# Kernel optimization log

Hardware: AMD Instinct MI355X
Metric: run time of the kernel (lower is better)

Reference implementation:

```python
import jax, jax.numpy as jnp
import numpy as np

B, D_IN, D_HID, D_OUT, E, TOP_K = 4096, 1024, 4096, 1024, 8, 2


def setup_inputs() -> dict:
    key = jax.random.key(0)
    ks = jax.random.split(key, 7)
    s_in = 1.0 / np.sqrt(D_IN)
    s_hid = 1.0 / np.sqrt(D_HID)
    return {
        "x": jax.random.normal(ks[0], (B, D_IN), jnp.float32),
        "Wg": jax.random.uniform(ks[1], (D_IN, E), jnp.float32, -s_in, s_in),
        "bg": jax.random.uniform(ks[2], (E,), jnp.float32, -s_in, s_in),
        "W1": jax.random.uniform(ks[3], (E, D_IN, D_HID), jnp.float32, -s_in, s_in),
        "b1": jax.random.uniform(ks[4], (E, D_HID), jnp.float32, -s_in, s_in),
        "W2": jax.random.uniform(ks[5], (E, D_HID, D_OUT), jnp.float32, -s_hid, s_hid),
        "b2": jax.random.uniform(ks[6], (E, D_OUT), jnp.float32, -s_hid, s_hid),
    }


def reference(x, Wg, bg, W1, b1, W2, b2):
    # Gating: [B, E]
    gate_logits = x @ Wg + bg
    # Top-k routing (values sorted descending, same as torch.topk)
    topk_logits, topk_idx = jax.lax.top_k(gate_logits, TOP_K)  # [B, K]
    topk_w = jax.nn.softmax(topk_logits, axis=-1)  # [B, K]

    # Dense per-expert FFN for all tokens (reference form of grouped GEMM)
    h = jax.nn.relu(jnp.einsum("bi,eih->beh", x, W1) + b1[None])  # [B, E, H]
    y = jnp.einsum("beh,eho->beo", h, W2) + b2[None]              # [B, E, O]

    # Gather selected experts' outputs and combine with routing weights
    y_sel = jnp.take_along_axis(y, topk_idx[:, :, None], axis=1)  # [B, K, O]
    output = jnp.sum(topk_w[:, :, None] * y_sel, axis=1)          # [B, O]

    # Load-balance auxiliary loss
    gates = jax.nn.softmax(gate_logits, axis=-1)
    expert_usage = gates.mean(axis=0)
    load_balance_loss = E * jnp.sum(expert_usage ** 2)
    return output, load_balance_loss
```

## Files before the change

kernel.cpp:

```cpp
#include <hip/hip_runtime.h>
#include <hip/hip_fp16.h>

#define BTOK  4096
#define D_IN  1024
#define D_HID 4096
#define D_OUT 1024
#define NE    8
#define PT_MAX 72
#define P_MAX  9216
#define HHALF  2048
#define KT1    32
#define NT1    16
#define KT2    64
#define NT2    8
#define GB     256

typedef _Float16 half8 __attribute__((ext_vector_type(8)));
typedef _Float16 half4v __attribute__((ext_vector_type(4)));
typedef float    floatx4 __attribute__((ext_vector_type(4)));


__device__ __forceinline__ void g2l16(const void* g, void* s) {
    __builtin_amdgcn_global_load_lds((const __attribute__((address_space(1))) void*)g,
                                     (__attribute__((address_space(3))) void*)s, 16, 0, 0);
}

__global__ __launch_bounds__(256)
void gating_kernel(const float* __restrict__ x, const float* __restrict__ Wg,
                   const float* __restrict__ bg,
                   int* __restrict__ t2i, float* __restrict__ t2w,
                   int* __restrict__ pcnt, float* __restrict__ pusage) {
    __shared__ float wgT[NE * 1024];
    __shared__ float susage[NE];
    __shared__ int   scnt[NE];
    int tid = threadIdx.x;
    if (tid < NE) { susage[tid] = 0.f; scnt[tid] = 0; }
    #pragma unroll
    for (int k = 0; k < 8192; k += 256) {
        int idx = k + tid;
        wgT[(idx & 7) * 1024 + (idx >> 3)] = Wg[idx];
    }
    __syncthreads();
    int wv = tid >> 6, lane = tid & 63;
    for (int tt = 0; tt < 4; ++tt) {
        int t = blockIdx.x * 16 + wv * 4 + tt;
        double part[NE];
        #pragma unroll
        for (int e = 0; e < NE; ++e) part[e] = 0.0;
        #pragma unroll
        for (int j = 0; j < 16; ++j) {
            int i = j * 64 + lane;
            double xv = (double)x[(size_t)t * D_IN + i];
            #pragma unroll
            for (int e = 0; e < NE; ++e) part[e] += xv * (double)wgT[e * 1024 + i];
        }
        #pragma unroll
        for (int e = 0; e < NE; ++e) {
            #pragma unroll
            for (int s = 32; s > 0; s >>= 1) part[e] += __shfl_xor(part[e], s, 64);
        }
        if (lane == 0) {
            float l[NE];
            #pragma unroll
            for (int e = 0; e < NE; ++e) l[e] = (float)part[e] + bg[e];
            float M = l[0];
            #pragma unroll
            for (int e = 1; e < NE; ++e) M = fmaxf(M, l[e]);
            float s = 0.f, g[NE];
            #pragma unroll
            for (int e = 0; e < NE; ++e) { g[e] = __expf(l[e] - M); s += g[e]; }
            float inv = 1.f / s;
            #pragma unroll
            for (int e = 0; e < NE; ++e) atomicAdd(&susage[e], g[e] * inv);
            int i0 = 0; float b0 = l[0];
            #pragma unroll
            for (int e = 1; e < NE; ++e) if (l[e] > b0) { b0 = l[e]; i0 = e; }
            int i1 = -1; float b1v = -1e30f;
            #pragma unroll
            for (int e = 0; e < NE; ++e) if (e != i0 && l[e] > b1v) { b1v = l[e]; i1 = e; }
            float w0 = 1.f / (1.f + expf(b1v - b0));
            t2i[2 * t] = i0; t2i[2 * t + 1] = i1;
            t2w[2 * t] = w0; t2w[2 * t + 1] = 1.f - w0;
            atomicAdd(&scnt[i0], 1);
            atomicAdd(&scnt[i1], 1);
        }
    }
    __syncthreads();
    if (tid < NE) {
        pcnt[blockIdx.x * NE + tid] = scnt[tid];
        pusage[blockIdx.x * NE + tid] = susage[tid];
    }
}

__global__ void scan_kernel(const int* __restrict__ pcnt, const float* __restrict__ pusage,
                            int* __restrict__ meta, float* __restrict__ out_loss) {
    int lane = threadIdx.x;
    int e = lane & 7, b0 = lane >> 3;
    int c = 0; float u = 0.f;
    for (int b = b0; b < GB; b += 8) { c += pcnt[b * 8 + e]; u += pusage[b * 8 + e]; }
    #pragma unroll
    for (int s = 8; s < 64; s <<= 1) { c += __shfl_xor(c, s, 64); u += __shfl_xor(u, s, 64); }
    int cAll[NE]; float uAll[NE];
    #pragma unroll
    for (int q = 0; q < NE; ++q) { cAll[q] = __shfl(c, q, 64); uAll[q] = __shfl(u, q, 64); }
    if (lane == 0) {
        int* cnt = meta; int* cursor = meta + 8; int* offs = meta + 16;
        int* tile2e = meta + 24; int* ntiles = meta + 96;
        int run = 0;
        for (int q = 0; q < NE; ++q) {
            cnt[q] = cAll[q];
            offs[q] = run; cursor[q] = run;
            int ntl = (cAll[q] + 127) >> 7;
            int tb = run >> 7;
            for (int i = 0; i < ntl; ++i) tile2e[tb + i] = q;
            run += ntl << 7;
        }
        ntiles[0] = run >> 7;
        float loss = 0.f;
        for (int q = 0; q < NE; ++q) { float uu = uAll[q] / (float)BTOK; loss += uu * uu; }
        out_loss[0] = (float)NE * loss;
    }
}

__global__ void fill_kernel(int* __restrict__ ptok) {
    ptok[blockIdx.x * 256 + threadIdx.x] = 0;
}

__global__ void scatter_kernel(const int* __restrict__ t2i, int* __restrict__ cursor,
                               int* __restrict__ ptok, int* __restrict__ pslot) {
    __shared__ int lcnt[NE], base[NE];
    int tid = threadIdx.x;
    if (tid < NE) lcnt[tid] = 0;
    __syncthreads();
    int t = blockIdx.x * 256 + tid;
    int e0 = t2i[2 * t], e1 = t2i[2 * t + 1];
    int l0 = atomicAdd(&lcnt[e0], 1);
    int l1 = atomicAdd(&lcnt[e1], 1);
    __syncthreads();
    if (tid < NE) base[tid] = atomicAdd(&cursor[tid], lcnt[tid]);
    __syncthreads();
    int s0 = base[e0] + l0, s1 = base[e1] + l1;
    ptok[s0] = t; ptok[s1] = t;
    pslot[2 * t] = s0; pslot[2 * t + 1] = s1;
}

__global__ void gather_x_kernel(const float* __restrict__ x, const int* __restrict__ ptok,
                                _Float16* __restrict__ xt) {
    int k0 = blockIdx.x, ptile = blockIdx.y;
    int t = threadIdx.x;
    int m = t >> 1, kb = (t & 1) * 16;
    int tok = ptok[ptile * 128 + m];
    const float* src = x + (size_t)tok * D_IN + k0 * 32 + kb;
    float4 v0 = *(const float4*)(src);
    float4 v1 = *(const float4*)(src + 4);
    float4 v2 = *(const float4*)(src + 8);
    float4 v3 = *(const float4*)(src + 12);
    half8 o0, o1;
    o0[0]=(_Float16)v0.x; o0[1]=(_Float16)v0.y; o0[2]=(_Float16)v0.z; o0[3]=(_Float16)v0.w;
    o0[4]=(_Float16)v1.x; o0[5]=(_Float16)v1.y; o0[6]=(_Float16)v1.z; o0[7]=(_Float16)v1.w;
    o1[0]=(_Float16)v2.x; o1[1]=(_Float16)v2.y; o1[2]=(_Float16)v2.z; o1[3]=(_Float16)v2.w;
    o1[4]=(_Float16)v3.x; o1[5]=(_Float16)v3.y; o1[6]=(_Float16)v3.z; o1[7]=(_Float16)v3.w;
    _Float16* dst = xt + ((size_t)ptile * KT1 + k0) * 4096 + t * 16;
    *(half8*)dst = o0;
    *(half8*)(dst + 8) = o1;
}

__global__ void wtile_kernel(const float* __restrict__ W, _Float16* __restrict__ Wt,
                             int Ktot, int Ntot, int k_off, int n_off, int KT, int NT) {
    int k0 = blockIdx.x, ntb = blockIdx.y, e = blockIdx.z;
    int t = threadIdx.x;
    int nl = t >> 1, kb = (t & 1) * 16;
    const float* src = W + ((size_t)e * Ktot + k_off + k0 * 32 + kb) * Ntot
                         + n_off + ntb * 128 + nl;
    float v[16];
    #pragma unroll
    for (int j = 0; j < 16; ++j) v[j] = src[(size_t)j * Ntot];
    half8 o0, o1;
    #pragma unroll
    for (int j = 0; j < 8; ++j) { o0[j] = (_Float16)v[j]; o1[j] = (_Float16)v[j + 8]; }
    _Float16* dst = Wt + (((size_t)e * NT + ntb) * KT + k0) * 4096 + t * 16;
    *(half8*)dst = o0;
    *(half8*)(dst + 8) = o1;
}

__global__ __launch_bounds__(256)
void gemm1_kernel(const _Float16* __restrict__ xt, const _Float16* __restrict__ W1t,
                  const float* __restrict__ b1, _Float16* __restrict__ ht,
                  const int* __restrict__ meta, int n_off) {
    int ptile = blockIdx.x;
    if (ptile >= meta[96]) return;
    int nt = blockIdx.y;
    int e = meta[24 + ptile];

    __shared__ __align__(16) _Float16 Asm[128 * 32];
    __shared__ __align__(16) _Float16 Bsm[128 * 32];

    int tid = threadIdx.x;
    int wave = tid >> 6, lane = tid & 63;
    const _Float16* Abase = xt + (size_t)ptile * KT1 * 4096;
    const _Float16* Bbase = W1t + ((size_t)(e * NT1 + nt) * KT1) * 4096;
    int stg = wave * 512 + lane * 8;

    floatx4 acc[4][4] = {};
    int lr = lane & 15, lq = lane >> 4;
    int wm = (wave & 1) * 64, wn = (wave >> 1) * 64;

    for (int k0 = 0; k0 < KT1; ++k0) {
        __syncthreads();
        const _Float16* aG = Abase + (size_t)k0 * 4096 + stg;
        const _Float16* bG = Bbase + (size_t)k0 * 4096 + stg;
        g2l16(aG,        &Asm[wave * 512]);
        g2l16(aG + 2048, &Asm[wave * 512 + 2048]);
        g2l16(bG,        &Bsm[wave * 512]);
        g2l16(bG + 2048, &Bsm[wave * 512 + 2048]);
        __syncthreads();
        half8 af[4], bf[4];
        #pragma unroll
        for (int f = 0; f < 4; ++f) {
            af[f] = *(const half8*)&Asm[(wm + f * 16 + lr) * 32 + lq * 8];
            bf[f] = *(const half8*)&Bsm[(wn + f * 16 + lr) * 32 + lq * 8];
        }
        #pragma unroll
        for (int mf = 0; mf < 4; ++mf)
            #pragma unroll
            for (int nf = 0; nf < 4; ++nf)
                acc[mf][nf] = __builtin_amdgcn_mfma_f32_16x16x32_f16(af[mf], bf[nf], acc[mf][nf], 0, 0, 0);
    }

    const float* b1e = b1 + (size_t)e * D_HID + n_off;
    #pragma unroll
    for (int mf = 0; mf < 4; ++mf) {
        #pragma unroll
        for (int v = 0; v < 4; ++v) {
            int m = wm + mf * 16 + lq * 4 + v;
            #pragma unroll
            for (int nf = 0; nf < 4; ++nf) {
                int hl = nt * 128 + wn + nf * 16 + lr;
                float val = acc[mf][nf][v] + b1e[hl];
                ht[((size_t)ptile * KT2 + (hl >> 5)) * 4096 + m * 32 + (hl & 31)]
                    = (_Float16)fmaxf(val, 0.f);
            }
        }
    }
}

__global__ __launch_bounds__(256)
void gemm2_kernel(const _Float16* __restrict__ ht, const _Float16* __restrict__ W2t,
                  _Float16* __restrict__ y, const int* __restrict__ meta) {
    int ptile = blockIdx.x;
    if (ptile >= meta[96]) return;
    int nt = blockIdx.y;
    int e = meta[24 + ptile];

    __shared__ __align__(16) _Float16 Asm[128 * 32];
    __shared__ __align__(16) _Float16 Bsm[128 * 32];

    int tid = threadIdx.x;
    int wave = tid >> 6, lane = tid & 63;
    const _Float16* Abase = ht + (size_t)ptile * KT2 * 4096;
    const _Float16* Bbase = W2t + ((size_t)(e * NT2 + nt) * KT2) * 4096;
    int stg = wave * 512 + lane * 8;

    floatx4 acc[4][4] = {};
    int lr = lane & 15, lq = lane >> 4;
    int wm = (wave & 1) * 64, wn = (wave >> 1) * 64;

    for (int k0 = 0; k0 < KT2; ++k0) {
        __syncthreads();
        const _Float16* aG = Abase + (size_t)k0 * 4096 + stg;
        const _Float16* bG = Bbase + (size_t)k0 * 4096 + stg;
        g2l16(aG,        &Asm[wave * 512]);
        g2l16(aG + 2048, &Asm[wave * 512 + 2048]);
        g2l16(bG,        &Bsm[wave * 512]);
        g2l16(bG + 2048, &Bsm[wave * 512 + 2048]);
        __syncthreads();
        half8 af[4], bf[4];
        #pragma unroll
        for (int f = 0; f < 4; ++f) {
            af[f] = *(const half8*)&Asm[(wm + f * 16 + lr) * 32 + lq * 8];
            bf[f] = *(const half8*)&Bsm[(wn + f * 16 + lr) * 32 + lq * 8];
        }
        #pragma unroll
        for (int mf = 0; mf < 4; ++mf)
            #pragma unroll
            for (int nf = 0; nf < 4; ++nf)
                acc[mf][nf] = __builtin_amdgcn_mfma_f32_16x16x32_f16(af[mf], bf[nf], acc[mf][nf], 0, 0, 0);
    }

    #pragma unroll
    for (int mf = 0; mf < 4; ++mf) {
        #pragma unroll
        for (int v = 0; v < 4; ++v) {
            int m = wm + mf * 16 + lq * 4 + v;
            #pragma unroll
            for (int nf = 0; nf < 4; ++nf) {
                int c = nt * 128 + wn + nf * 16 + lr;
                y[(size_t)(ptile * 128 + m) * D_OUT + c] = (_Float16)acc[mf][nf][v];
            }
        }
    }
}

__global__ void combine_kernel(const _Float16* __restrict__ yA, const _Float16* __restrict__ yB,
                               const float* __restrict__ b2, const int* __restrict__ t2i,
                               const float* __restrict__ t2w, const int* __restrict__ pslot,
                               float* __restrict__ out) {
    int t = blockIdx.x;
    int c = threadIdx.x * 4;
    int e0 = t2i[2 * t], e1 = t2i[2 * t + 1];
    float w0 = t2w[2 * t], w1 = t2w[2 * t + 1];
    size_t s0 = (size_t)pslot[2 * t] * D_OUT + c;
    size_t s1 = (size_t)pslot[2 * t + 1] * D_OUT + c;
    half4v a0 = *(const half4v*)(yA + s0);
    half4v b0 = *(const half4v*)(yB + s0);
    half4v a1 = *(const half4v*)(yA + s1);
    half4v b1v = *(const half4v*)(yB + s1);
    float4 bias0 = *(const float4*)(b2 + (size_t)e0 * D_OUT + c);
    float4 bias1 = *(const float4*)(b2 + (size_t)e1 * D_OUT + c);
    float4 o;
    o.x = w0 * ((float)a0[0] + (float)b0[0] + bias0.x) + w1 * ((float)a1[0] + (float)b1v[0] + bias1.x);
    o.y = w0 * ((float)a0[1] + (float)b0[1] + bias0.y) + w1 * ((float)a1[1] + (float)b1v[1] + bias1.y);
    o.z = w0 * ((float)a0[2] + (float)b0[2] + bias0.z) + w1 * ((float)a1[2] + (float)b1v[2] + bias1.z);
    o.w = w0 * ((float)a0[3] + (float)b0[3] + bias0.w) + w1 * ((float)a1[3] + (float)b1v[3] + bias1.w);
    *(float4*)(out + (size_t)t * D_OUT + c) = o;
}

extern "C" void kernel_launch(void* const* d_in, const int* in_sizes, int n_in,
                              void* d_out, int out_size, void* d_ws, size_t ws_size,
                              hipStream_t stream) {
    const float* x  = (const float*)d_in[0];
    const float* Wg = (const float*)d_in[1];
    const float* bg = (const float*)d_in[2];
    const float* W1 = (const float*)d_in[3];
    const float* b1 = (const float*)d_in[4];
    const float* W2 = (const float*)d_in[5];
    const float* b2 = (const float*)d_in[6];
    float* out = (float*)d_out;

    char* ws = (char*)d_ws;
    _Float16* xt     = (_Float16*)(ws);
    _Float16* Wt     = (_Float16*)(ws + 18874368ull);
    _Float16* ht     = (_Float16*)(ws + 52428800ull);
    _Float16* yA     = (_Float16*)(ws + 90177536ull);
    _Float16* yB     = (_Float16*)(ws + 109051904ull);
    int*      t2i    = (int*)(ws + 127926272ull);
    float*    t2w    = (float*)(ws + 127959040ull);
    int*      ptok   = (int*)(ws + 127991808ull);
    int*      pslot  = (int*)(ws + 128028672ull);
    int*      meta   = (int*)(ws + 128061440ull);
    int*      pcnt   = (int*)(ws + 128061952ull);
    float*    pusage = (float*)(ws + 128070144ull);
    int* cursor = meta + 8;

    hipMemsetAsync(meta, 0, 512, stream);

    gating_kernel<<<GB, 256, 0, stream>>>(x, Wg, bg, t2i, t2w, pcnt, pusage);
    scan_kernel<<<1, 64, 0, stream>>>(pcnt, pusage, meta, out + (size_t)BTOK * D_OUT);
    fill_kernel<<<36, 256, 0, stream>>>(ptok);
    scatter_kernel<<<16, 256, 0, stream>>>(t2i, cursor, ptok, pslot);
    gather_x_kernel<<<dim3(KT1, PT_MAX), 256, 0, stream>>>(x, ptok, xt);

    wtile_kernel<<<dim3(KT1, NT1, 8), 256, 0, stream>>>(W1, Wt, D_IN, D_HID, 0, 0, KT1, NT1);
    gemm1_kernel<<<dim3(PT_MAX, NT1), 256, 0, stream>>>(xt, Wt, b1, ht, meta, 0);
    wtile_kernel<<<dim3(KT2, NT2, 8), 256, 0, stream>>>(W2, Wt, D_HID, D_OUT, 0, 0, KT2, NT2);
    gemm2_kernel<<<dim3(PT_MAX, NT2), 256, 0, stream>>>(ht, Wt, yA, meta);

    wtile_kernel<<<dim3(KT1, NT1, 8), 256, 0, stream>>>(W1, Wt, D_IN, D_HID, 0, HHALF, KT1, NT1);
    gemm1_kernel<<<dim3(PT_MAX, NT1), 256, 0, stream>>>(xt, Wt, b1, ht, meta, HHALF);
    wtile_kernel<<<dim3(KT2, NT2, 8), 256, 0, stream>>>(W2, Wt, D_HID, D_OUT, HHALF, 0, KT2, NT2);
    gemm2_kernel<<<dim3(PT_MAX, NT2), 256, 0, stream>>>(ht, Wt, yB, meta);

    combine_kernel<<<BTOK, 256, 0, stream>>>(yA, yB, b2, t2i, t2w, pslot, out);
}
```

Before: 585.2 us.

## Double-buffer GEMM LDS tiles and merge split hidden-dimension passes

```diff
diff --git a/kernel.cpp b/kernel.cpp
--- a/kernel.cpp
+++ b/kernel.cpp
@@ -8,12 +8,11 @@
 #define NE    8
 #define PT_MAX 72
 #define P_MAX  9216
-#define HHALF  2048
-#define KT1    32
-#define NT1    16
-#define KT2    64
-#define NT2    8
-#define GB     256
+#define KT1   32
+#define NT1M  32
+#define KT2M  128
+#define NT2   8
+#define GB    256
 
 typedef _Float16 half8 __attribute__((ext_vector_type(8)));
 typedef _Float16 half4v __attribute__((ext_vector_type(4)));
@@ -166,12 +165,11 @@
 }
 
 __global__ void wtile_kernel(const float* __restrict__ W, _Float16* __restrict__ Wt,
-                             int Ktot, int Ntot, int k_off, int n_off, int KT, int NT) {
+                             int Ktot, int Ntot, int KT, int NT) {
     int k0 = blockIdx.x, ntb = blockIdx.y, e = blockIdx.z;
     int t = threadIdx.x;
     int nl = t >> 1, kb = (t & 1) * 16;
-    const float* src = W + ((size_t)e * Ktot + k_off + k0 * 32 + kb) * Ntot
-                         + n_off + ntb * 128 + nl;
+    const float* src = W + ((size_t)e * Ktot + k0 * 32 + kb) * Ntot + ntb * 128 + nl;
     float v[16];
     #pragma unroll
     for (int j = 0; j < 16; ++j) v[j] = src[(size_t)j * Ntot];
@@ -183,51 +181,63 @@
     *(half8*)(dst + 8) = o1;
 }
 
-__global__ __launch_bounds__(256)
+__global__ __launch_bounds__(256, 3)
 void gemm1_kernel(const _Float16* __restrict__ xt, const _Float16* __restrict__ W1t,
                   const float* __restrict__ b1, _Float16* __restrict__ ht,
-                  const int* __restrict__ meta, int n_off) {
+                  const int* __restrict__ meta) {
     int ptile = blockIdx.x;
     if (ptile >= meta[96]) return;
     int nt = blockIdx.y;
     int e = meta[24 + ptile];
 
-    __shared__ __align__(16) _Float16 Asm[128 * 32];
-    __shared__ __align__(16) _Float16 Bsm[128 * 32];
+    __shared__ __align__(16) _Float16 Asm[2][128 * 32];
+    __shared__ __align__(16) _Float16 Bsm[2][128 * 32];
 
     int tid = threadIdx.x;
     int wave = tid >> 6, lane = tid & 63;
     const _Float16* Abase = xt + (size_t)ptile * KT1 * 4096;
-    const _Float16* Bbase = W1t + ((size_t)(e * NT1 + nt) * KT1) * 4096;
+    const _Float16* Bbase = W1t + ((size_t)(e * NT1M + nt) * KT1) * 4096;
     int stg = wave * 512 + lane * 8;
 
     floatx4 acc[4][4] = {};
     int lr = lane & 15, lq = lane >> 4;
     int wm = (wave & 1) * 64, wn = (wave >> 1) * 64;
 
+    g2l16(Abase + stg,        &Asm[0][wave * 512]);
+    g2l16(Abase + stg + 2048, &Asm[0][wave * 512 + 2048]);
+    g2l16(Bbase + stg,        &Bsm[0][wave * 512]);
+    g2l16(Bbase + stg + 2048, &Bsm[0][wave * 512 + 2048]);
+    __syncthreads();
+
+    int ct = 0;
     for (int k0 = 0; k0 < KT1; ++k0) {
-        __syncthreads();
-        const _Float16* aG = Abase + (size_t)k0 * 4096 + stg;
-        const _Float16* bG = Bbase + (size_t)k0 * 4096 + stg;
-        g2l16(aG,        &Asm[wave * 512]);
-        g2l16(aG + 2048, &Asm[wave * 512 + 2048]);
-        g2l16(bG,        &Bsm[wave * 512]);
-        g2l16(bG + 2048, &Bsm[wave * 512 + 2048]);
-        __syncthreads();
+        if (k0 + 1 < KT1) {
+            const _Float16* aG = Abase + (size_t)(k0 + 1) * 4096 + stg;
+            const _Float16* bG = Bbase + (size_t)(k0 + 1) * 4096 + stg;
+            int nb = ct ^ 1;
+            g2l16(aG,        &Asm[nb][wave * 512]);
+            g2l16(aG + 2048, &Asm[nb][wave * 512 + 2048]);
+            g2l16(bG,        &Bsm[nb][wave * 512]);
+            g2l16(bG + 2048, &Bsm[nb][wave * 512 + 2048]);
+        }
+        const _Float16* As = Asm[ct];
+        const _Float16* Bs = Bsm[ct];
         half8 af[4], bf[4];
         #pragma unroll
         for (int f = 0; f < 4; ++f) {
-            af[f] = *(const half8*)&Asm[(wm + f * 16 + lr) * 32 + lq * 8];
-            bf[f] = *(const half8*)&Bsm[(wn + f * 16 + lr) * 32 + lq * 8];
+            af[f] = *(const half8*)&As[(wm + f * 16 + lr) * 32 + lq * 8];
+            bf[f] = *(const half8*)&Bs[(wn + f * 16 + lr) * 32 + lq * 8];
         }
         #pragma unroll
         for (int mf = 0; mf < 4; ++mf)
             #pragma unroll
             for (int nf = 0; nf < 4; ++nf)
                 acc[mf][nf] = __builtin_amdgcn_mfma_f32_16x16x32_f16(af[mf], bf[nf], acc[mf][nf], 0, 0, 0);
-    }
-
-    const float* b1e = b1 + (size_t)e * D_HID + n_off;
+        __syncthreads();
+        ct ^= 1;
+    }
+
+    const float* b1e = b1 + (size_t)e * D_HID;
     #pragma unroll
     for (int mf = 0; mf < 4; ++mf) {
         #pragma unroll
@@ -237,14 +247,14 @@
             for (int nf = 0; nf < 4; ++nf) {
                 int hl = nt * 128 + wn + nf * 16 + lr;
                 float val = acc[mf][nf][v] + b1e[hl];
-                ht[((size_t)ptile * KT2 + (hl >> 5)) * 4096 + m * 32 + (hl & 31)]
+                ht[((size_t)ptile * KT2M + (hl >> 5)) * 4096 + m * 32 + (hl & 31)]
                     = (_Float16)fmaxf(val, 0.f);
             }
         }
     }
 }
 
-__global__ __launch_bounds__(256)
+__global__ __launch_bounds__(256, 3)
 void gemm2_kernel(const _Float16* __restrict__ ht, const _Float16* __restrict__ W2t,
                   _Float16* __restrict__ y, const int* __restrict__ meta) {
     int ptile = blockIdx.x;
@@ -252,39 +262,51 @@
     int nt = blockIdx.y;
     int e = meta[24 + ptile];
 
-    __shared__ __align__(16) _Float16 Asm[128 * 32];
-    __shared__ __align__(16) _Float16 Bsm[128 * 32];
+    __shared__ __align__(16) _Float16 Asm[2][128 * 32];
+    __shared__ __align__(16) _Float16 Bsm[2][128 * 32];
 
     int tid = threadIdx.x;
     int wave = tid >> 6, lane = tid & 63;
-    const _Float16* Abase = ht + (size_t)ptile * KT2 * 4096;
-    const _Float16* Bbase = W2t + ((size_t)(e * NT2 + nt) * KT2) * 4096;
+    const _Float16* Abase = ht + (size_t)ptile * KT2M * 4096;
+    const _Float16* Bbase = W2t + ((size_t)(e * NT2 + nt) * KT2M) * 4096;
     int stg = wave * 512 + lane * 8;
 
     floatx4 acc[4][4] = {};
     int lr = lane & 15, lq = lane >> 4;
     int wm = (wave & 1) * 64, wn = (wave >> 1) * 64;
 
-    for (int k0 = 0; k0 < KT2; ++k0) {
-        __syncthreads();
-        const _Float16* aG = Abase + (size_t)k0 * 4096 + stg;
-        const _Float16* bG = Bbase + (size_t)k0 * 4096 + stg;
-        g2l16(aG,        &Asm[wave * 512]);
-        g2l16(aG + 2048, &Asm[wave * 512 + 2048]);
-        g2l16(bG,        &Bsm[wave * 512]);
-        g2l16(bG + 2048, &Bsm[wave * 512 + 2048]);
-        __syncthreads();
+    g2l16(Abase + stg,        &Asm[0][wave * 512]);
+    g2l16(Abase + stg + 2048, &Asm[0][wave * 512 + 2048]);
+    g2l16(Bbase + stg,        &Bsm[0][wave * 512]);
+    g2l16(Bbase + stg + 2048, &Bsm[0][wave * 512 + 2048]);
+    __syncthreads();
+
+    int ct = 0;
+    for (int k0 = 0; k0 < KT2M; ++k0) {
+        if (k0 + 1 < KT2M) {
+            const _Float16* aG = Abase + (size_t)(k0 + 1) * 4096 + stg;
+            const _Float16* bG = Bbase + (size_t)(k0 + 1) * 4096 + stg;
+            int nb = ct ^ 1;
+            g2l16(aG,        &Asm[nb][wave * 512]);
+            g2l16(aG + 2048, &Asm[nb][wave * 512 + 2048]);
+            g2l16(bG,        &Bsm[nb][wave * 512]);
+            g2l16(bG + 2048, &Bsm[nb][wave * 512 + 2048]);
+        }
+        const _Float16* As = Asm[ct];
+        const _Float16* Bs = Bsm[ct];
         half8 af[4], bf[4];
         #pragma unroll
         for (int f = 0; f < 4; ++f) {
-            af[f] = *(const half8*)&Asm[(wm + f * 16 + lr) * 32 + lq * 8];
-            bf[f] = *(const half8*)&Bsm[(wn + f * 16 + lr) * 32 + lq * 8];
+            af[f] = *(const half8*)&As[(wm + f * 16 + lr) * 32 + lq * 8];
+            bf[f] = *(const half8*)&Bs[(wn + f * 16 + lr) * 32 + lq * 8];
         }
         #pragma unroll
         for (int mf = 0; mf < 4; ++mf)
             #pragma unroll
             for (int nf = 0; nf < 4; ++nf)
                 acc[mf][nf] = __builtin_amdgcn_mfma_f32_16x16x32_f16(af[mf], bf[nf], acc[mf][nf], 0, 0, 0);
+        __syncthreads();
+        ct ^= 1;
     }
 
     #pragma unroll
@@ -301,27 +323,24 @@
     }
 }
 
-__global__ void combine_kernel(const _Float16* __restrict__ yA, const _Float16* __restrict__ yB,
-                               const float* __restrict__ b2, const int* __restrict__ t2i,
-                               const float* __restrict__ t2w, const int* __restrict__ pslot,
-                               float* __restrict__ out) {
+__global__ void combine_kernel(const _Float16* __restrict__ y, const float* __restrict__ b2,
+                               const int* __restrict__ t2i, const float* __restrict__ t2w,
+                               const int* __restrict__ pslot, float* __restrict__ out) {
     int t = blockIdx.x;
     int c = threadIdx.x * 4;
     int e0 = t2i[2 * t], e1 = t2i[2 * t + 1];
     float w0 = t2w[2 * t], w1 = t2w[2 * t + 1];
     size_t s0 = (size_t)pslot[2 * t] * D_OUT + c;
     size_t s1 = (size_t)pslot[2 * t + 1] * D_OUT + c;
-    half4v a0 = *(const half4v*)(yA + s0);
-    half4v b0 = *(const half4v*)(yB + s0);
-    half4v a1 = *(const half4v*)(yA + s1);
-    half4v b1v = *(const half4v*)(yB + s1);
+    half4v a0 = *(const half4v*)(y + s0);
+    half4v a1 = *(const half4v*)(y + s1);
     float4 bias0 = *(const float4*)(b2 + (size_t)e0 * D_OUT + c);
     float4 bias1 = *(const float4*)(b2 + (size_t)e1 * D_OUT + c);
     float4 o;
-    o.x = w0 * ((float)a0[0] + (float)b0[0] + bias0.x) + w1 * ((float)a1[0] + (float)b1v[0] + bias1.x);
-    o.y = w0 * ((float)a0[1] + (float)b0[1] + bias0.y) + w1 * ((float)a1[1] + (float)b1v[1] + bias1.y);
-    o.z = w0 * ((float)a0[2] + (float)b0[2] + bias0.z) + w1 * ((float)a1[2] + (float)b1v[2] + bias1.z);
-    o.w = w0 * ((float)a0[3] + (float)b0[3] + bias0.w) + w1 * ((float)a1[3] + (float)b1v[3] + bias1.w);
+    o.x = w0 * ((float)a0[0] + bias0.x) + w1 * ((float)a1[0] + bias1.x);
+    o.y = w0 * ((float)a0[1] + bias0.y) + w1 * ((float)a1[1] + bias1.y);
+    o.z = w0 * ((float)a0[2] + bias0.z) + w1 * ((float)a1[2] + bias1.z);
+    o.w = w0 * ((float)a0[3] + bias0.w) + w1 * ((float)a1[3] + bias1.w);
     *(float4*)(out + (size_t)t * D_OUT + c) = o;
 }
 
@@ -339,17 +358,17 @@
 
     char* ws = (char*)d_ws;
     _Float16* xt     = (_Float16*)(ws);
-    _Float16* Wt     = (_Float16*)(ws + 18874368ull);
-    _Float16* ht     = (_Float16*)(ws + 52428800ull);
-    _Float16* yA     = (_Float16*)(ws + 90177536ull);
-    _Float16* yB     = (_Float16*)(ws + 109051904ull);
-    int*      t2i    = (int*)(ws + 127926272ull);
-    float*    t2w    = (float*)(ws + 127959040ull);
-    int*      ptok   = (int*)(ws + 127991808ull);
-    int*      pslot  = (int*)(ws + 128028672ull);
-    int*      meta   = (int*)(ws + 128061440ull);
-    int*      pcnt   = (int*)(ws + 128061952ull);
-    float*    pusage = (float*)(ws + 128070144ull);
+    _Float16* W1t    = (_Float16*)(ws + 18874368ull);
+    _Float16* W2t    = (_Float16*)(ws + 85983232ull);
+    _Float16* ht     = (_Float16*)(ws + 153092096ull);
+    _Float16* y      = (_Float16*)(ws + 228589568ull);
+    int*      t2i    = (int*)(ws + 247463936ull);
+    float*    t2w    = (float*)(ws + 247496704ull);
+    int*      ptok   = (int*)(ws + 247529472ull);
+    int*      pslot  = (int*)(ws + 247566336ull);
+    int*      meta   = (int*)(ws + 247599104ull);
+    int*      pcnt   = (int*)(ws + 247599616ull);
+    float*    pusage = (float*)(ws + 247607808ull);
     int* cursor = meta + 8;
 
     hipMemsetAsync(meta, 0, 512, stream);
@@ -360,15 +379,11 @@
     scatter_kernel<<<16, 256, 0, stream>>>(t2i, cursor, ptok, pslot);
     gather_x_kernel<<<dim3(KT1, PT_MAX), 256, 0, stream>>>(x, ptok, xt);
 
-    wtile_kernel<<<dim3(KT1, NT1, 8), 256, 0, stream>>>(W1, Wt, D_IN, D_HID, 0, 0, KT1, NT1);
-    gemm1_kernel<<<dim3(PT_MAX, NT1), 256, 0, stream>>>(xt, Wt, b1, ht, meta, 0);
-    wtile_kernel<<<dim3(KT2, NT2, 8), 256, 0, stream>>>(W2, Wt, D_HID, D_OUT, 0, 0, KT2, NT2);
-    gemm2_kernel<<<dim3(PT_MAX, NT2), 256, 0, stream>>>(ht, Wt, yA, meta);
-
-    wtile_kernel<<<dim3(KT1, NT1, 8), 256, 0, stream>>>(W1, Wt, D_IN, D_HID, 0, HHALF, KT1, NT1);
-    gemm1_kernel<<<dim3(PT_MAX, NT1), 256, 0, stream>>>(xt, Wt, b1, ht, meta, HHALF);
-    wtile_kernel<<<dim3(KT2, NT2, 8), 256, 0, stream>>>(W2, Wt, D_HID, D_OUT, HHALF, 0, KT2, NT2);
-    gemm2_kernel<<<dim3(PT_MAX, NT2), 256, 0, stream>>>(ht, Wt, yB, meta);
-
-    combine_kernel<<<BTOK, 256, 0, stream>>>(yA, yB, b2, t2i, t2w, pslot, out);
-}
+    wtile_kernel<<<dim3(KT1, NT1M, 8), 256, 0, stream>>>(W1, W1t, D_IN, D_HID, KT1, NT1M);
+    wtile_kernel<<<dim3(KT2M, NT2, 8), 256, 0, stream>>>(W2, W2t, D_HID, D_OUT, KT2M, NT2);
+
+    gemm1_kernel<<<dim3(PT_MAX, NT1M), 256, 0, stream>>>(xt, W1t, b1, ht, meta);
+    gemm2_kernel<<<dim3(PT_MAX, NT2), 256, 0, stream>>>(ht, W2t, y, meta);
+
+    combine_kernel<<<BTOK, 256, 0, stream>>>(y, b2, t2i, t2w, pslot, out);
+}
```

New measurement: 602.6 us. 3.0% more time.
